# Kernel optimization log

Measured on AMD Instinct MI355X. Metric: run time of the kernel, lower is better.

## Reference

```python
import itertools
import jax, jax.numpy as jnp
import numpy as np

N = 9   # rows; N! = 362880 permutations
D = 512 # feature dim


def setup_inputs() -> dict:
    key = jax.random.key(0)
    k_x, k_w1, k_w2 = jax.random.split(key, 3)
    x = jax.random.normal(k_x, (N, D), dtype=jnp.float32)
    # nn.Linear-style init scale
    W1 = jax.random.normal(k_w1, (D, 32), dtype=jnp.float32) / np.sqrt(D)
    b1 = jnp.zeros((32,), dtype=jnp.float32)
    W2 = jax.random.normal(k_w2, (32, 4), dtype=jnp.float32) / np.sqrt(32)
    b2 = jnp.zeros((4,), dtype=jnp.float32)
    # exact permutation table the torch loop iterates (itertools order)
    perms = jnp.asarray(
        np.array(list(itertools.permutations(range(N))), dtype=np.int32)
    )  # [N!, N]
    return {"x": x, "W1": W1, "b1": b1, "W2": W2, "b2": b2, "perms": perms}


def reference(x, W1, b1, W2, b2, perms):
    # linear(x[perm]) == linear(x)[perm] since the MLP acts rowwise,
    # so compute the MLP once and accumulate gathered rows over all perms.
    y = jnp.maximum(x @ W1 + b1, 0.0) @ W2 + b2          # [N, 4]
    gathered = jnp.take(y, perms, axis=0)                 # [N!, N, 4]
    return gathered.sum(axis=0)                           # [N, 4]
```

## Files before the change

### kernel.cpp

```cpp
#include <hip/hip_runtime.h>


#define NROWS 9
#define DDIM  512
#define HDIM  32
#define OUTC  4
#define NBLK  64
#define DPB   (DDIM / NBLK)
#define NPAIR (NROWS * HDIM)
#define FACT8 40320.0f

__global__ __launch_bounds__(NPAIR)
void sym_partial_kernel(const float* __restrict__ x,
                        const float* __restrict__ W1,
                        float* __restrict__ part)
{
    const int t  = threadIdx.x;
    const int i  = t >> 5;
    const int h  = t & 31;
    const int d0 = blockIdx.x * DPB;

    const float4* x4 = (const float4*)(x + i * DDIM + d0);
    const float4 xa = x4[0];
    const float4 xb = x4[1];

    float w[DPB];
#pragma unroll
    for (int k = 0; k < DPB; ++k) w[k] = W1[(d0 + k) * HDIM + h];

    float s = (xa.x * w[0] + xa.y * w[1]) + (xa.z * w[2] + xa.w * w[3])
            + (xb.x * w[4] + xb.y * w[5]) + (xb.z * w[6] + xb.w * w[7]);

    part[blockIdx.x * NPAIR + t] = s;
}

__global__ __launch_bounds__(NPAIR)
void sym_finish_kernel(const float* __restrict__ part,
                       const float* __restrict__ b1,
                       const float* __restrict__ W2,
                       const float* __restrict__ b2,
                       float* __restrict__ out)
{
    __shared__ float hbuf[NROWS][HDIM];
    __shared__ float hsum[HDIM];

    const int t = threadIdx.x;
    const int i = t >> 5;
    const int h = t & 31;

    float s0 = 0.f, s1 = 0.f, s2 = 0.f, s3 = 0.f;
#pragma unroll
    for (int b = 0; b < NBLK; b += 4) {
        s0 += part[(b + 0) * NPAIR + t];
        s1 += part[(b + 1) * NPAIR + t];
        s2 += part[(b + 2) * NPAIR + t];
        s3 += part[(b + 3) * NPAIR + t];
    }
    const float hv = (s0 + s1) + (s2 + s3) + b1[h];
    hbuf[i][h] = hv > 0.f ? hv : 0.f;
    __syncthreads();

    if (t < HDIM) {
        float s = 0.f;
#pragma unroll
        for (int r = 0; r < NROWS; ++r) s += hbuf[r][t];
        hsum[t] = s;
    }
    __syncthreads();

    if (t < NROWS * OUTC) {
        const int c = t & 3;
        float s = 0.f;
#pragma unroll
        for (int hh = 0; hh < HDIM; ++hh) s += hsum[hh] * W2[hh * OUTC + c];
        out[t] = FACT8 * (s + (float)NROWS * b2[c]);
    }
}

extern "C" void kernel_launch(void* const* d_in, const int* in_sizes, int n_in,
                              void* d_out, int out_size, void* d_ws, size_t ws_size,
                              hipStream_t stream)
{
    const float* x  = (const float*)d_in[0];
    const float* W1 = (const float*)d_in[1];
    const float* b1 = (const float*)d_in[2];
    const float* W2 = (const float*)d_in[3];
    const float* b2 = (const float*)d_in[4];
    float* out  = (float*)d_out;
    float* part = (float*)d_ws;

    sym_partial_kernel<<<NBLK, NPAIR, 0, stream>>>(x, W1, part);
    sym_finish_kernel<<<1, NPAIR, 0, stream>>>(part, b1, W2, b2, out);
}
```

Measured before the change: 70.81 us.

## Fuse partial and finish kernels into one single-block kernel with shared-memory reduction

Replaces the two-kernel scheme (64 blocks writing partial sums to workspace, then a single-block finish kernel) with one 1024-thread block. Each thread holds a 16-element slice of W1 in registers, computes dot products for all 9 rows, and the partials are reduced in shared memory before the ReLU and W2 stage. This removes a kernel launch and the global-memory round trip for the partials. In exchange all work runs on a single CU with less parallelism for loading x and W1.

```diff
diff --git a/kernel.cpp b/kernel.cpp
--- a/kernel.cpp
+++ b/kernel.cpp
@@ -5,59 +5,59 @@
 #define DDIM  512
 #define HDIM  32
 #define OUTC  4
-#define NBLK  64
-#define DPB   (DDIM / NBLK)
-#define NPAIR (NROWS * HDIM)
+#define NCH   32
+#define DCH   (DDIM / NCH)
+#define NTHR  (NCH * HDIM)
 #define FACT8 40320.0f
 
-__global__ __launch_bounds__(NPAIR)
-void sym_partial_kernel(const float* __restrict__ x,
-                        const float* __restrict__ W1,
-                        float* __restrict__ part)
+__global__ __launch_bounds__(NTHR)
+void sym_all_kernel(const float* __restrict__ x,
+                    const float* __restrict__ W1,
+                    const float* __restrict__ b1,
+                    const float* __restrict__ W2,
+                    const float* __restrict__ b2,
+                    float* __restrict__ out)
 {
-    const int t  = threadIdx.x;
-    const int i  = t >> 5;
-    const int h  = t & 31;
-    const int d0 = blockIdx.x * DPB;
-
-    const float4* x4 = (const float4*)(x + i * DDIM + d0);
-    const float4 xa = x4[0];
-    const float4 xb = x4[1];
-
-    float w[DPB];
-#pragma unroll
-    for (int k = 0; k < DPB; ++k) w[k] = W1[(d0 + k) * HDIM + h];
-
-    float s = (xa.x * w[0] + xa.y * w[1]) + (xa.z * w[2] + xa.w * w[3])
-            + (xb.x * w[4] + xb.y * w[5]) + (xb.z * w[6] + xb.w * w[7]);
-
-    part[blockIdx.x * NPAIR + t] = s;
-}
-
-__global__ __launch_bounds__(NPAIR)
-void sym_finish_kernel(const float* __restrict__ part,
-                       const float* __restrict__ b1,
-                       const float* __restrict__ W2,
-                       const float* __restrict__ b2,
-                       float* __restrict__ out)
-{
+    __shared__ float part[NROWS][NCH][HDIM];
     __shared__ float hbuf[NROWS][HDIM];
     __shared__ float hsum[HDIM];
 
-    const int t = threadIdx.x;
-    const int i = t >> 5;
-    const int h = t & 31;
+    const int t  = threadIdx.x;
+    const int h  = t & 31;
+    const int c0 = t >> 5;
+    const int d0 = c0 * DCH;
 
-    float s0 = 0.f, s1 = 0.f, s2 = 0.f, s3 = 0.f;
+    float w[DCH];
 #pragma unroll
-    for (int b = 0; b < NBLK; b += 4) {
-        s0 += part[(b + 0) * NPAIR + t];
-        s1 += part[(b + 1) * NPAIR + t];
-        s2 += part[(b + 2) * NPAIR + t];
-        s3 += part[(b + 3) * NPAIR + t];
+    for (int k = 0; k < DCH; ++k) w[k] = W1[(d0 + k) * HDIM + h];
+
+#pragma unroll
+    for (int i = 0; i < NROWS; ++i) {
+        const float4* x4 = (const float4*)(x + i * DDIM + d0);
+        float acc = 0.f;
+#pragma unroll
+        for (int q = 0; q < DCH / 4; ++q) {
+            const float4 v = x4[q];
+            acc += (v.x * w[4*q+0] + v.y * w[4*q+1])
+                 + (v.z * w[4*q+2] + v.w * w[4*q+3]);
+        }
+        part[i][c0][h] = acc;
     }
-    const float hv = (s0 + s1) + (s2 + s3) + b1[h];
-    hbuf[i][h] = hv > 0.f ? hv : 0.f;
+    __syncthreads();
+
+    if (t < NROWS * HDIM) {
+        const int i = t >> 5;
+        float s0 = 0.f, s1 = 0.f, s2 = 0.f, s3 = 0.f;
+#pragma unroll
+        for (int cc = 0; cc < NCH; cc += 4) {
+            s0 += part[i][cc + 0][h];
+            s1 += part[i][cc + 1][h];
+            s2 += part[i][cc + 2][h];
+            s3 += part[i][cc + 3][h];
+        }
+        const float hv = (s0 + s1) + (s2 + s3) + b1[h];
+        hbuf[i][h] = hv > 0.f ? hv : 0.f;
+    }
     __syncthreads();
 
     if (t < HDIM) {
@@ -86,9 +86,7 @@
     const float* b1 = (const float*)d_in[2];
     const float* W2 = (const float*)d_in[3];
     const float* b2 = (const float*)d_in[4];
-    float* out  = (float*)d_out;
-    float* part = (float*)d_ws;
+    float* out = (float*)d_out;
 
-    sym_partial_kernel<<<NBLK, NPAIR, 0, stream>>>(x, W1, part);
-    sym_finish_kernel<<<1, NPAIR, 0, stream>>>(part, b1, W2, b2, out);
+    sym_all_kernel<<<1, NTHR, 0, stream>>>(x, W1, b1, W2, b2, out);
 }
```

Measured after the change: 74.64 us. +5.4%, slower.
